# Performance work log

Hardware: AMD Instinct MI355X
Metric: run time of the kernel (lower is better)

The kernel has to match this reference:

```python
import jax, jax.numpy as jnp
import numpy as np

OSC_TIME = 10
UNITS = 256
D_IN = 256
BATCH = 32
SEQLEN = 2000


def setup_inputs() -> dict:
    key = jax.random.key(0)
    k1, k2, k3 = jax.random.split(key, 3)
    scale = 1.0 / np.sqrt(UNITS)
    x = jax.random.normal(k1, (BATCH, SEQLEN, D_IN), dtype=jnp.float32)
    W_x = jax.random.normal(k2, (4, 2, D_IN, UNITS), dtype=jnp.float32) * scale
    W_h = jax.random.normal(k3, (4, 2, UNITS, UNITS), dtype=jnp.float32) * scale
    b_x = jnp.zeros((4, 2, UNITS), dtype=jnp.float32)
    b_h = jnp.zeros((4, 2, UNITS), dtype=jnp.float32)
    return {"x": x, "W_x": W_x, "b_x": b_x, "W_h": W_h, "b_h": b_h}


def reference(x, W_x, b_x, W_h, b_h):
    # Subsample every OSC_TIME steps (tf.gather stride)
    xs = x[:, ::OSC_TIME]                       # [B, Ts, D]
    B, Ts, _ = xs.shape
    U = W_h.shape[-1]

    # Precompute input projections for all 4 cells x 2 gates: [4,2,B,Ts,U]
    xp = jnp.einsum('btd,cgdu->cgbtu', xs, W_x) + b_x[:, :, None, None, :]

    h0 = jnp.zeros((4, B, U), dtype=x.dtype)

    def ff_step(h, xp_t):                       # h [4,B,U], xp_t [4,2,B,U]
        hp = jnp.einsum('cbu,cguv->cgbv', h, W_h) + b_h[:, :, None, :]
        g = jax.nn.sigmoid(xp_t + hp)           # [4,2,B,U]
        j, k = g[:, 0], g[:, 1]
        h_new = j * (1.0 - h) + (1.0 - k) * h   # flip-flop update
        return h_new, h_new

    _, hs = jax.lax.scan(ff_step, h0, jnp.moveaxis(xp, 3, 0))  # hs [Ts,4,B,U]
    phi, omega, r, mu = hs[:, 0], hs[:, 1], hs[:, 2], hs[:, 3]  # each [Ts,B,U]

    # Oscillator: emit z = r*cos(phi) then update r, phi; OSC_TIME sub-steps
    def osc_step(carry, _):
        r_t, phi_t = carry
        z = r_t * jnp.cos(phi_t)
        r_n = r_t + (mu - jnp.square(r_t)) * r_t
        phi_n = phi_t + omega
        return (r_n, phi_n), z

    _, zs = jax.lax.scan(osc_step, (r, phi), None, length=OSC_TIME)  # [S,Ts,B,U]
    out = jnp.transpose(zs, (2, 1, 0, 3)).reshape(B, Ts * OSC_TIME, U)
    return out
```

## Files before the change

kernel.cpp:

```cpp
#include <hip/hip_runtime.h>
#include <hip/hip_fp16.h>
#include <stdint.h>

#define TS 200

typedef _Float16 h2_t  __attribute__((ext_vector_type(2)));
typedef _Float16 f16x8 __attribute__((ext_vector_type(8)));
typedef float    f32x4 __attribute__((ext_vector_type(4)));

static __device__ __forceinline__ float fdot2f(uint32_t w, uint32_t h, float acc) {
#if __has_builtin(__builtin_amdgcn_fdot2)
    return __builtin_amdgcn_fdot2(__builtin_bit_cast(h2_t, w),
                                  __builtin_bit_cast(h2_t, h), acc, false);
#else
    h2_t a = __builtin_bit_cast(h2_t, w), b = __builtin_bit_cast(h2_t, h);
    acc = fmaf((float)a.x, (float)b.x, acc);
    acc = fmaf((float)a.y, (float)b.y, acc);
    return acc;
#endif
}

template <int CTRL>
static __device__ __forceinline__ float dpp_add(float x) {
    int m = __builtin_amdgcn_update_dpp(0, __builtin_bit_cast(int, x), CTRL, 0xF, 0xF, true);
    return x + __builtin_bit_cast(float, m);
}
template <int CTRL>
static __device__ __forceinline__ float dpp_mov(float x) {
    int m = __builtin_amdgcn_update_dpp(0, __builtin_bit_cast(int, x), CTRL, 0xF, 0xF, true);
    return __builtin_bit_cast(float, m);
}

__global__ __launch_bounds__(256) void pack_all(const float* __restrict__ x,
                                                const float* __restrict__ Wx,
                                                const float* __restrict__ Wh,
                                                _Float16* __restrict__ xh,
                                                _Float16* __restrict__ wxt,
                                                uint32_t* __restrict__ wp) {
    int bid = blockIdx.x, tid = threadIdx.x;
    if (bid < 6400) {
        int row = bid, col = tid;
        int b = row / 200, t = row - b * 200;
        xh[(size_t)row * 256 + col] = (_Float16)x[((size_t)(b * 2000 + t * 10)) * 256 + col];
    } else if (bid < 8448) {
        int n = bid - 6400, k = tid;
        wxt[(size_t)n * 256 + k] = (_Float16)Wx[((size_t)((n >> 8) * 256 + k)) * 256 + (n & 255)];
    } else {
        int idx = (bid - 8448) * 256 + tid;
        int e   = idx & 3;
        int thr = (idx >> 2) & 1023;
        int j   = (idx >> 12) & 15;
        int c   = idx >> 16;
        int a = j >> 2, i = j & 3;
        int uu = a >> 1, g = a & 1;
        int vs = thr & 7, uq = (thr >> 3) & 7, wv = thr >> 6;
        int u = (wv * 8 + uq) * 2 + uu;
        int v = vs * 32 + i * 8 + e * 2;
        const float* base = Wh + ((size_t)((c * 2 + g) * 256 + v)) * 256 + u;
        h2_t p; p.x = (_Float16)base[0]; p.y = (_Float16)base[256];
        wp[idx] = __builtin_bit_cast(uint32_t, p);
    }
}

__global__ __launch_bounds__(256) void xp_gemm(const _Float16* __restrict__ xh,
                                               const _Float16* __restrict__ wxt,
                                               const float* __restrict__ bxf,
                                               _Float16* __restrict__ xp) {
    __shared__ _Float16 As[128 * 64];
    __shared__ _Float16 Bs[128 * 64];
    const int tid = threadIdx.x;
    const int lane = tid & 63, w = tid >> 6;
    const int m0 = (blockIdx.x >> 4) * 128;
    const int n0 = (blockIdx.x & 15) * 128;
    const int mw = (w & 1) * 64, nw = (w >> 1) * 64;

    f32x4 acc[4][4] = {};

    for (int kb = 0; kb < 4; kb++) {
        const int k0 = kb * 64;
#pragma unroll
        for (int q = 0; q < 4; q++) {
            int ii = w * 4 + q;
            int r = ii * 8 + (lane >> 3);
            int kcol = (lane & 7) * 8;
            const _Float16* ga = xh  + (size_t)(m0 + r) * 256 + k0 + kcol;
            const _Float16* gb = wxt + (size_t)(n0 + r) * 256 + k0 + kcol;
            __builtin_amdgcn_global_load_lds(
                (const __attribute__((address_space(1))) uint32_t*)ga,
                (__attribute__((address_space(3))) uint32_t*)(As + ii * 512), 16, 0, 0);
            __builtin_amdgcn_global_load_lds(
                (const __attribute__((address_space(1))) uint32_t*)gb,
                (__attribute__((address_space(3))) uint32_t*)(Bs + ii * 512), 16, 0, 0);
        }
        __syncthreads();
#pragma unroll
        for (int kc = 0; kc < 2; kc++) {
            f16x8 a[4], b[4];
#pragma unroll
            for (int mt = 0; mt < 4; mt++)
                a[mt] = *(const f16x8*)&As[(mw + mt * 16 + (lane & 15)) * 64 + kc * 32 + (lane >> 4) * 8];
#pragma unroll
            for (int nt = 0; nt < 4; nt++)
                b[nt] = *(const f16x8*)&Bs[(nw + nt * 16 + (lane & 15)) * 64 + kc * 32 + (lane >> 4) * 8];
#pragma unroll
            for (int mt = 0; mt < 4; mt++)
#pragma unroll
                for (int nt = 0; nt < 4; nt++)
                    acc[mt][nt] = __builtin_amdgcn_mfma_f32_16x16x32_f16(a[mt], b[nt], acc[mt][nt], 0, 0, 0);
        }
        __syncthreads();
    }

    const int nl = lane & 15, quad = lane >> 4;
#pragma unroll
    for (int nt = 0; nt < 4; nt++) {
        int n = n0 + nw + nt * 16 + nl;
        float bias = bxf[n];
        int c = n >> 9, gu = n & 511;
#pragma unroll
        for (int mt = 0; mt < 4; mt++)
#pragma unroll
            for (int r = 0; r < 4; r++) {
                int m = m0 + mw + mt * 16 + quad * 4 + r;
                int b = m / 200, t = m - b * 200;
                xp[((size_t)((c * 32 + b) * 200 + t)) * 512 + gu] =
                    (_Float16)(acc[mt][nt][r] + bias);
            }
    }
}

#define D4(ACC, W, H)                 \
    ACC = fdot2f(W.x, H.x, ACC);      \
    ACC = fdot2f(W.y, H.y, ACC);      \
    ACC = fdot2f(W.z, H.z, ACC);      \
    ACC = fdot2f(W.w, H.w, ACC);

#define PIN4(W) asm volatile("" : "+v"(W.x), "+v"(W.y), "+v"(W.z), "+v"(W.w))

__global__ __attribute__((amdgpu_flat_work_group_size(1024, 1024),
                          amdgpu_waves_per_eu(4, 4)))
void recurrence(const _Float16* __restrict__ xp,
                const float* __restrict__ bh,
                const uint32_t* __restrict__ Wp,
                float* __restrict__ hs) {
    const int cb  = blockIdx.x;
    const int c   = cb >> 5;
    const int tid = threadIdx.x;
    const int lane = tid & 63;
    const int vs = lane & 7;
    const int uq = lane >> 3;
    const int wv = tid >> 6;
    const int upair = wv * 8 + uq;
    const int u0 = upair * 2;

    __shared__ __align__(16) uint32_t h2s[2][160];

    const uint4* wb = (const uint4*)Wp + (size_t)c * 16 * 1024 + tid;
    uint4 w00 = wb[0 * 1024],  w01 = wb[1 * 1024],  w02 = wb[2 * 1024],  w03 = wb[3 * 1024];
    uint4 w10 = wb[4 * 1024],  w11 = wb[5 * 1024],  w12 = wb[6 * 1024],  w13 = wb[7 * 1024];
    uint4 w20 = wb[8 * 1024],  w21 = wb[9 * 1024],  w22 = wb[10 * 1024], w23 = wb[11 * 1024];
    uint4 w30 = wb[12 * 1024], w31 = wb[13 * 1024], w32 = wb[14 * 1024], w33 = wb[15 * 1024];
    PIN4(w00); PIN4(w01); PIN4(w02); PIN4(w03);
    PIN4(w10); PIN4(w11); PIN4(w12); PIN4(w13);
    PIN4(w20); PIN4(w21); PIN4(w22); PIN4(w23);
    PIN4(w30); PIN4(w31); PIN4(w32); PIN4(w33);

    float bias = 0.f;
    const _Float16* xpb = nullptr;
    if (vs < 4) {
        int g_sel = vs & 1, u_sel = u0 + (vs >> 1);
        bias = bh[(c * 2 + g_sel) * 256 + u_sel];
        xpb  = xp + (size_t)cb * 200 * 512 + g_sel * 256 + u_sel;
    }

    float hreg = 0.f;
    if (tid < 160) { h2s[0][tid] = 0u; }
    __syncthreads();

    float* hsb = hs + (size_t)cb * 200 * 256 + u0;

    for (int t = 0; t < TS; t++) {
        const uint32_t* hbuf = h2s[t & 1];
        uint32_t* hnext = h2s[(t + 1) & 1];

        float xpv = 0.f;
        if (vs < 4) xpv = (float)xpb[(size_t)t * 512];

        uint4 h0 = *(const uint4*)(hbuf + vs * 20 + 0);
        uint4 h1 = *(const uint4*)(hbuf + vs * 20 + 4);
        uint4 h2 = *(const uint4*)(hbuf + vs * 20 + 8);
        uint4 h3 = *(const uint4*)(hbuf + vs * 20 + 12);

        float acc0 = 0.f, acc1 = 0.f, acc2 = 0.f, acc3 = 0.f;
        D4(acc0, w00, h0) D4(acc1, w10, h0) D4(acc2, w20, h0) D4(acc3, w30, h0)
        D4(acc0, w01, h1) D4(acc1, w11, h1) D4(acc2, w21, h1) D4(acc3, w31, h1)
        D4(acc0, w02, h2) D4(acc1, w12, h2) D4(acc2, w22, h2) D4(acc3, w32, h2)
        D4(acc0, w03, h3) D4(acc1, w13, h3) D4(acc2, w23, h3) D4(acc3, w33, h3)

        acc0 = dpp_add<0x141>(dpp_add<0x4E>(dpp_add<0xB1>(acc0)));
        acc1 = dpp_add<0x141>(dpp_add<0x4E>(dpp_add<0xB1>(acc1)));
        acc2 = dpp_add<0x141>(dpp_add<0x4E>(dpp_add<0xB1>(acc2)));
        acc3 = dpp_add<0x141>(dpp_add<0x4E>(dpp_add<0xB1>(acc3)));

        float s = (vs == 0) ? acc0 : (vs == 1) ? acc1 : (vs == 2) ? acc2 : acc3;
        s += xpv + bias;
        float sig = 1.f / (1.f + __expf(-s));
        float kg = dpp_mov<0xB1>(sig);
        float hn = sig + hreg * (1.f - sig - kg);
        hreg = hn;
        float hn1 = dpp_mov<0x4E>(hn);
        if (vs == 0) {
            h2_t p; p.x = (_Float16)hn; p.y = (_Float16)hn1;
            hnext[(upair >> 4) * 20 + (upair & 15)] = __builtin_bit_cast(uint32_t, p);
            *(float2*)(hsb + (size_t)t * 256) = make_float2(hn, hn1);
        }
        __syncthreads();
    }
}

__global__ __launch_bounds__(256) void osc(const float* __restrict__ hs,
                                           float* __restrict__ out) {
    int tid = blockIdx.x * 256 + threadIdx.x;
    const int cstride = 32 * 200 * 256;
    int u = tid & 255;
    int bt = tid >> 8;
    int t = bt % 200, b = bt / 200;
    float phi   = hs[0 * cstride + tid];
    float omega = hs[1 * cstride + tid];
    float r     = hs[2 * cstride + tid];
    float mu    = hs[3 * cstride + tid];
    float* o = out + ((size_t)(b * 2000 + t * 10)) * 256 + u;
#pragma unroll
    for (int s = 0; s < 10; s++) {
        o[(size_t)s * 256] = r * __cosf(phi);
        r = r + (mu - r * r) * r;
        phi = phi + omega;
    }
}

extern "C" void kernel_launch(void* const* d_in, const int* in_sizes, int n_in,
                              void* d_out, int out_size, void* d_ws, size_t ws_size,
                              hipStream_t stream) {
    const float* x  = (const float*)d_in[0];
    const float* Wx = (const float*)d_in[1];
    const float* bx = (const float*)d_in[2];
    const float* Wh = (const float*)d_in[3];
    const float* bh = (const float*)d_in[4];
    float* out = (float*)d_out;

    char* ws = (char*)d_ws;
    const size_t XP = (size_t)4 * 32 * 200 * 512 * 2;
    const size_t HS = (size_t)4 * 32 * 200 * 256 * 4;
    const size_t XH = (size_t)6400 * 256 * 2;

    _Float16* xp  = (_Float16*)ws;
    float*    hs  = (float*)(ws + XP);
    _Float16* xh  = (_Float16*)(ws + XP);
    _Float16* wxt = (_Float16*)(ws + XP + XH);
    uint32_t* wp  = (uint32_t*)(ws + XP + HS);

    pack_all<<<9472, 256, 0, stream>>>(x, Wx, Wh, xh, wxt, wp);
    xp_gemm<<<800, 256, 0, stream>>>(xh, wxt, bx, xp);
    recurrence<<<128, 1024, 0, stream>>>(xp, bh, wp, hs);
    osc<<<6400, 256, 0, stream>>>(hs, out);
}
```

Measured before the change: 374.0 us.

## Halve recurrence block size, each thread computes two unit-pairs

The recurrence kernel now launches 512 threads per block instead of 1024, and each thread holds two sets of weight registers (A and B halves, 128 units apart). Each thread does twice the dot-product work per timestep. The aim is to reduce per-step barrier cost and wave count across the serial loop, and to add ILP by interleaving independent accumulations. In exchange, register pressure doubles, with 128 pinned weight VGPRs plus accumulators, which could cause spills or lower occupancy limits.

```diff
diff --git a/kernel.cpp b/kernel.cpp
--- a/kernel.cpp
+++ b/kernel.cpp
@@ -137,8 +137,8 @@
 
 #define PIN4(W) asm volatile("" : "+v"(W.x), "+v"(W.y), "+v"(W.z), "+v"(W.w))
 
-__global__ __attribute__((amdgpu_flat_work_group_size(1024, 1024),
-                          amdgpu_waves_per_eu(4, 4)))
+__global__ __attribute__((amdgpu_flat_work_group_size(512, 512),
+                          amdgpu_waves_per_eu(2, 2)))
 void recurrence(const _Float16* __restrict__ xp,
                 const float* __restrict__ bh,
                 const uint32_t* __restrict__ Wp,
@@ -150,30 +150,39 @@
     const int vs = lane & 7;
     const int uq = lane >> 3;
     const int wv = tid >> 6;
-    const int upair = wv * 8 + uq;
-    const int u0 = upair * 2;
+    const int up0 = wv * 8 + uq;
+    const int u0 = up0 * 2;
 
     __shared__ __align__(16) uint32_t h2s[2][160];
 
     const uint4* wb = (const uint4*)Wp + (size_t)c * 16 * 1024 + tid;
-    uint4 w00 = wb[0 * 1024],  w01 = wb[1 * 1024],  w02 = wb[2 * 1024],  w03 = wb[3 * 1024];
-    uint4 w10 = wb[4 * 1024],  w11 = wb[5 * 1024],  w12 = wb[6 * 1024],  w13 = wb[7 * 1024];
-    uint4 w20 = wb[8 * 1024],  w21 = wb[9 * 1024],  w22 = wb[10 * 1024], w23 = wb[11 * 1024];
-    uint4 w30 = wb[12 * 1024], w31 = wb[13 * 1024], w32 = wb[14 * 1024], w33 = wb[15 * 1024];
-    PIN4(w00); PIN4(w01); PIN4(w02); PIN4(w03);
-    PIN4(w10); PIN4(w11); PIN4(w12); PIN4(w13);
-    PIN4(w20); PIN4(w21); PIN4(w22); PIN4(w23);
-    PIN4(w30); PIN4(w31); PIN4(w32); PIN4(w33);
-
-    float bias = 0.f;
+    uint4 wA00 = wb[0 * 1024],        wA01 = wb[1 * 1024],        wA02 = wb[2 * 1024],        wA03 = wb[3 * 1024];
+    uint4 wA10 = wb[4 * 1024],        wA11 = wb[5 * 1024],        wA12 = wb[6 * 1024],        wA13 = wb[7 * 1024];
+    uint4 wA20 = wb[8 * 1024],        wA21 = wb[9 * 1024],        wA22 = wb[10 * 1024],       wA23 = wb[11 * 1024];
+    uint4 wA30 = wb[12 * 1024],       wA31 = wb[13 * 1024],       wA32 = wb[14 * 1024],       wA33 = wb[15 * 1024];
+    uint4 wB00 = wb[0 * 1024 + 512],  wB01 = wb[1 * 1024 + 512],  wB02 = wb[2 * 1024 + 512],  wB03 = wb[3 * 1024 + 512];
+    uint4 wB10 = wb[4 * 1024 + 512],  wB11 = wb[5 * 1024 + 512],  wB12 = wb[6 * 1024 + 512],  wB13 = wb[7 * 1024 + 512];
+    uint4 wB20 = wb[8 * 1024 + 512],  wB21 = wb[9 * 1024 + 512],  wB22 = wb[10 * 1024 + 512], wB23 = wb[11 * 1024 + 512];
+    uint4 wB30 = wb[12 * 1024 + 512], wB31 = wb[13 * 1024 + 512], wB32 = wb[14 * 1024 + 512], wB33 = wb[15 * 1024 + 512];
+    PIN4(wA00); PIN4(wA01); PIN4(wA02); PIN4(wA03);
+    PIN4(wA10); PIN4(wA11); PIN4(wA12); PIN4(wA13);
+    PIN4(wA20); PIN4(wA21); PIN4(wA22); PIN4(wA23);
+    PIN4(wA30); PIN4(wA31); PIN4(wA32); PIN4(wA33);
+    PIN4(wB00); PIN4(wB01); PIN4(wB02); PIN4(wB03);
+    PIN4(wB10); PIN4(wB11); PIN4(wB12); PIN4(wB13);
+    PIN4(wB20); PIN4(wB21); PIN4(wB22); PIN4(wB23);
+    PIN4(wB30); PIN4(wB31); PIN4(wB32); PIN4(wB33);
+
+    float biasA = 0.f, biasB = 0.f;
     const _Float16* xpb = nullptr;
     if (vs < 4) {
         int g_sel = vs & 1, u_sel = u0 + (vs >> 1);
-        bias = bh[(c * 2 + g_sel) * 256 + u_sel];
+        biasA = bh[(c * 2 + g_sel) * 256 + u_sel];
+        biasB = bh[(c * 2 + g_sel) * 256 + u_sel + 128];
         xpb  = xp + (size_t)cb * 200 * 512 + g_sel * 256 + u_sel;
     }
 
-    float hreg = 0.f;
+    float hregA = 0.f, hregB = 0.f;
     if (tid < 160) { h2s[0][tid] = 0u; }
     __syncthreads();
 
@@ -183,36 +192,59 @@
         const uint32_t* hbuf = h2s[t & 1];
         uint32_t* hnext = h2s[(t + 1) & 1];
 
-        float xpv = 0.f;
-        if (vs < 4) xpv = (float)xpb[(size_t)t * 512];
+        float xpA = 0.f, xpB = 0.f;
+        if (vs < 4) {
+            xpA = (float)xpb[(size_t)t * 512];
+            xpB = (float)xpb[(size_t)t * 512 + 128];
+        }
 
         uint4 h0 = *(const uint4*)(hbuf + vs * 20 + 0);
         uint4 h1 = *(const uint4*)(hbuf + vs * 20 + 4);
         uint4 h2 = *(const uint4*)(hbuf + vs * 20 + 8);
         uint4 h3 = *(const uint4*)(hbuf + vs * 20 + 12);
 
-        float acc0 = 0.f, acc1 = 0.f, acc2 = 0.f, acc3 = 0.f;
-        D4(acc0, w00, h0) D4(acc1, w10, h0) D4(acc2, w20, h0) D4(acc3, w30, h0)
-        D4(acc0, w01, h1) D4(acc1, w11, h1) D4(acc2, w21, h1) D4(acc3, w31, h1)
-        D4(acc0, w02, h2) D4(acc1, w12, h2) D4(acc2, w22, h2) D4(acc3, w32, h2)
-        D4(acc0, w03, h3) D4(acc1, w13, h3) D4(acc2, w23, h3) D4(acc3, w33, h3)
-
-        acc0 = dpp_add<0x141>(dpp_add<0x4E>(dpp_add<0xB1>(acc0)));
-        acc1 = dpp_add<0x141>(dpp_add<0x4E>(dpp_add<0xB1>(acc1)));
-        acc2 = dpp_add<0x141>(dpp_add<0x4E>(dpp_add<0xB1>(acc2)));
-        acc3 = dpp_add<0x141>(dpp_add<0x4E>(dpp_add<0xB1>(acc3)));
-
-        float s = (vs == 0) ? acc0 : (vs == 1) ? acc1 : (vs == 2) ? acc2 : acc3;
-        s += xpv + bias;
-        float sig = 1.f / (1.f + __expf(-s));
-        float kg = dpp_mov<0xB1>(sig);
-        float hn = sig + hreg * (1.f - sig - kg);
-        hreg = hn;
-        float hn1 = dpp_mov<0x4E>(hn);
+        float aA0 = 0.f, aA1 = 0.f, aA2 = 0.f, aA3 = 0.f;
+        float aB0 = 0.f, aB1 = 0.f, aB2 = 0.f, aB3 = 0.f;
+        D4(aA0, wA00, h0) D4(aB0, wB00, h0) D4(aA1, wA10, h0) D4(aB1, wB10, h0)
+        D4(aA2, wA20, h0) D4(aB2, wB20, h0) D4(aA3, wA30, h0) D4(aB3, wB30, h0)
+        D4(aA0, wA01, h1) D4(aB0, wB01, h1) D4(aA1, wA11, h1) D4(aB1, wB11, h1)
+        D4(aA2, wA21, h1) D4(aB2, wB21, h1) D4(aA3, wA31, h1) D4(aB3, wB31, h1)
+        D4(aA0, wA02, h2) D4(aB0, wB02, h2) D4(aA1, wA12, h2) D4(aB1, wB12, h2)
+        D4(aA2, wA22, h2) D4(aB2, wB22, h2) D4(aA3, wA32, h2) D4(aB3, wB32, h2)
+        D4(aA0, wA03, h3) D4(aB0, wB03, h3) D4(aA1, wA13, h3) D4(aB1, wB13, h3)
+        D4(aA2, wA23, h3) D4(aB2, wB23, h3) D4(aA3, wA33, h3) D4(aB3, wB33, h3)
+
+        aA0 = dpp_add<0x141>(dpp_add<0x4E>(dpp_add<0xB1>(aA0)));
+        aA1 = dpp_add<0x141>(dpp_add<0x4E>(dpp_add<0xB1>(aA1)));
+        aA2 = dpp_add<0x141>(dpp_add<0x4E>(dpp_add<0xB1>(aA2)));
+        aA3 = dpp_add<0x141>(dpp_add<0x4E>(dpp_add<0xB1>(aA3)));
+        aB0 = dpp_add<0x141>(dpp_add<0x4E>(dpp_add<0xB1>(aB0)));
+        aB1 = dpp_add<0x141>(dpp_add<0x4E>(dpp_add<0xB1>(aB1)));
+        aB2 = dpp_add<0x141>(dpp_add<0x4E>(dpp_add<0xB1>(aB2)));
+        aB3 = dpp_add<0x141>(dpp_add<0x4E>(dpp_add<0xB1>(aB3)));
+
+        float sA = (vs == 0) ? aA0 : (vs == 1) ? aA1 : (vs == 2) ? aA2 : aA3;
+        float sB = (vs == 0) ? aB0 : (vs == 1) ? aB1 : (vs == 2) ? aB2 : aB3;
+        sA += xpA + biasA;
+        sB += xpB + biasB;
+        float sigA = 1.f / (1.f + __expf(-sA));
+        float sigB = 1.f / (1.f + __expf(-sB));
+        float kgA = dpp_mov<0xB1>(sigA);
+        float kgB = dpp_mov<0xB1>(sigB);
+        float hnA = sigA + hregA * (1.f - sigA - kgA);
+        float hnB = sigB + hregB * (1.f - sigB - kgB);
+        hregA = hnA;
+        hregB = hnB;
+        float hn1A = dpp_mov<0x4E>(hnA);
+        float hn1B = dpp_mov<0x4E>(hnB);
         if (vs == 0) {
-            h2_t p; p.x = (_Float16)hn; p.y = (_Float16)hn1;
-            hnext[(upair >> 4) * 20 + (upair & 15)] = __builtin_bit_cast(uint32_t, p);
-            *(float2*)(hsb + (size_t)t * 256) = make_float2(hn, hn1);
+            h2_t pA; pA.x = (_Float16)hnA; pA.y = (_Float16)hn1A;
+            h2_t pB; pB.x = (_Float16)hnB; pB.y = (_Float16)hn1B;
+            int idx0 = (up0 >> 4) * 20 + (up0 & 15);
+            hnext[idx0]      = __builtin_bit_cast(uint32_t, pA);
+            hnext[idx0 + 80] = __builtin_bit_cast(uint32_t, pB);
+            *(float2*)(hsb + (size_t)t * 256)       = make_float2(hnA, hn1A);
+            *(float2*)(hsb + (size_t)t * 256 + 128) = make_float2(hnB, hn1B);
         }
         __syncthreads();
     }
@@ -261,6 +293,6 @@
 
     pack_all<<<9472, 256, 0, stream>>>(x, Wx, Wh, xh, wxt, wp);
     xp_gemm<<<800, 256, 0, stream>>>(xh, wxt, bx, xp);
-    recurrence<<<128, 1024, 0, stream>>>(xp, bh, wp, hs);
+    recurrence<<<128, 512, 0, stream>>>(xp, bh, wp, hs);
     osc<<<6400, 256, 0, stream>>>(hs, out);
 }
```

Measured after the change: 381.2 us. About the same (+1.9%).

## Batch recurrence across 16 sequences per workgroup using MFMA with register-resident weights

Applied to the files above, without the earlier changes.

The recurrence kernel now processes 16 batch rows per workgroup. Each step's h·W_h product runs as 16x16x32 f16 MFMA tiles against weights pinned in registers, replacing per-sequence fdot2 dot products with DPP reductions. The h state is exchanged through XOR-swizzled LDS, the next step's xp values are prefetched, and the barrier becomes a lighter LDS-only one. Weight packing is rewritten to the MFMA operand layout. The grid shrinks from 128 to 8 workgroups, trading parallelism across CUs for far fewer weight loads and matrix-core throughput, so per-step latency on only 8 CUs may dominate.

```diff
diff --git a/kernel.cpp b/kernel.cpp
--- a/kernel.cpp
+++ b/kernel.cpp
@@ -7,28 +7,11 @@
 typedef _Float16 h2_t  __attribute__((ext_vector_type(2)));
 typedef _Float16 f16x8 __attribute__((ext_vector_type(8)));
 typedef float    f32x4 __attribute__((ext_vector_type(4)));
-
-static __device__ __forceinline__ float fdot2f(uint32_t w, uint32_t h, float acc) {
-#if __has_builtin(__builtin_amdgcn_fdot2)
-    return __builtin_amdgcn_fdot2(__builtin_bit_cast(h2_t, w),
-                                  __builtin_bit_cast(h2_t, h), acc, false);
-#else
-    h2_t a = __builtin_bit_cast(h2_t, w), b = __builtin_bit_cast(h2_t, h);
-    acc = fmaf((float)a.x, (float)b.x, acc);
-    acc = fmaf((float)a.y, (float)b.y, acc);
-    return acc;
-#endif
-}
 
 template <int CTRL>
 static __device__ __forceinline__ float dpp_add(float x) {
     int m = __builtin_amdgcn_update_dpp(0, __builtin_bit_cast(int, x), CTRL, 0xF, 0xF, true);
     return x + __builtin_bit_cast(float, m);
-}
-template <int CTRL>
-static __device__ __forceinline__ float dpp_mov(float x) {
-    int m = __builtin_amdgcn_update_dpp(0, __builtin_bit_cast(int, x), CTRL, 0xF, 0xF, true);
-    return __builtin_bit_cast(float, m);
 }
 
 __global__ __launch_bounds__(256) void pack_all(const float* __restrict__ x,
@@ -36,7 +19,7 @@
                                                 const float* __restrict__ Wh,
                                                 _Float16* __restrict__ xh,
                                                 _Float16* __restrict__ wxt,
-                                                uint32_t* __restrict__ wp) {
+                                                _Float16* __restrict__ wp) {
     int bid = blockIdx.x, tid = threadIdx.x;
     if (bid < 6400) {
         int row = bid, col = tid;
@@ -46,19 +29,17 @@
         int n = bid - 6400, k = tid;
         wxt[(size_t)n * 256 + k] = (_Float16)Wx[((size_t)((n >> 8) * 256 + k)) * 256 + (n & 255)];
     } else {
-        int idx = (bid - 8448) * 256 + tid;
-        int e   = idx & 3;
-        int thr = (idx >> 2) & 1023;
-        int j   = (idx >> 12) & 15;
-        int c   = idx >> 16;
-        int a = j >> 2, i = j & 3;
-        int uu = a >> 1, g = a & 1;
-        int vs = thr & 7, uq = (thr >> 3) & 7, wv = thr >> 6;
-        int u = (wv * 8 + uq) * 2 + uu;
-        int v = vs * 32 + i * 8 + e * 2;
-        const float* base = Wh + ((size_t)((c * 2 + g) * 256 + v)) * 256 + u;
-        h2_t p; p.x = (_Float16)base[0]; p.y = (_Float16)base[256];
-        wp[idx] = __builtin_bit_cast(uint32_t, p);
+        int i = (bid - 8448) * 256 + tid;
+        int e  = i & 7;
+        int ln = (i >> 3) & 63;
+        int kt = (i >> 9) & 7;
+        int nt = (i >> 12) & 3;
+        int w  = (i >> 14) & 7;
+        int c  = i >> 17;
+        int g = nt >> 1, par = nt & 1;
+        int u = w * 32 + 2 * (ln & 15) + par;
+        int k = kt * 32 + (ln >> 4) * 8 + e;
+        wp[i] = (_Float16)Wh[((size_t)((c * 2 + g) * 256 + k)) * 256 + u];
     }
 }
 
@@ -129,92 +110,130 @@
     }
 }
 
-#define D4(ACC, W, H)                 \
-    ACC = fdot2f(W.x, H.x, ACC);      \
-    ACC = fdot2f(W.y, H.y, ACC);      \
-    ACC = fdot2f(W.z, H.z, ACC);      \
-    ACC = fdot2f(W.w, H.w, ACC);
-
 #define PIN4(W) asm volatile("" : "+v"(W.x), "+v"(W.y), "+v"(W.z), "+v"(W.w))
 
-__global__ __attribute__((amdgpu_flat_work_group_size(1024, 1024),
-                          amdgpu_waves_per_eu(4, 4)))
+#define LDS_BARRIER()                                        \
+    do {                                                     \
+        __builtin_amdgcn_sched_barrier(0);                   \
+        asm volatile("s_waitcnt lgkmcnt(0)" ::: "memory");   \
+        __builtin_amdgcn_s_barrier();                        \
+        __builtin_amdgcn_sched_barrier(0);                   \
+    } while (0)
+
+__global__ __attribute__((amdgpu_flat_work_group_size(512, 512),
+                          amdgpu_waves_per_eu(2, 2)))
 void recurrence(const _Float16* __restrict__ xp,
                 const float* __restrict__ bh,
-                const uint32_t* __restrict__ Wp,
+                const _Float16* __restrict__ Wp,
                 float* __restrict__ hs) {
-    const int cb  = blockIdx.x;
-    const int c   = cb >> 5;
+    const int wg  = blockIdx.x;
+    const int c   = wg >> 1;
+    const int bb  = wg & 1;
     const int tid = threadIdx.x;
     const int lane = tid & 63;
-    const int vs = lane & 7;
-    const int uq = lane >> 3;
-    const int wv = tid >> 6;
-    const int upair = wv * 8 + uq;
-    const int u0 = upair * 2;
-
-    __shared__ __align__(16) uint32_t h2s[2][160];
-
-    const uint4* wb = (const uint4*)Wp + (size_t)c * 16 * 1024 + tid;
-    uint4 w00 = wb[0 * 1024],  w01 = wb[1 * 1024],  w02 = wb[2 * 1024],  w03 = wb[3 * 1024];
-    uint4 w10 = wb[4 * 1024],  w11 = wb[5 * 1024],  w12 = wb[6 * 1024],  w13 = wb[7 * 1024];
-    uint4 w20 = wb[8 * 1024],  w21 = wb[9 * 1024],  w22 = wb[10 * 1024], w23 = wb[11 * 1024];
-    uint4 w30 = wb[12 * 1024], w31 = wb[13 * 1024], w32 = wb[14 * 1024], w33 = wb[15 * 1024];
-    PIN4(w00); PIN4(w01); PIN4(w02); PIN4(w03);
-    PIN4(w10); PIN4(w11); PIN4(w12); PIN4(w13);
-    PIN4(w20); PIN4(w21); PIN4(w22); PIN4(w23);
-    PIN4(w30); PIN4(w31); PIN4(w32); PIN4(w33);
-
-    float bias = 0.f;
-    const _Float16* xpb = nullptr;
-    if (vs < 4) {
-        int g_sel = vs & 1, u_sel = u0 + (vs >> 1);
-        bias = bh[(c * 2 + g_sel) * 256 + u_sel];
-        xpb  = xp + (size_t)cb * 200 * 512 + g_sel * 256 + u_sel;
-    }
-
-    float hreg = 0.f;
-    if (tid < 160) { h2s[0][tid] = 0u; }
+    const int w    = tid >> 6;
+    const int c16  = lane & 15;
+    const int quad = lane >> 4;
+    const int ub   = w * 32;
+
+    __shared__ __align__(16) char hb[2][16 * 512];
+
+    uint4 W[4][8];
+    {
+        const uint4* wq = (const uint4*)Wp;
+        const int base = ((c * 8 + w) * 4) * 8 * 64;
+#pragma unroll
+        for (int nt = 0; nt < 4; nt++)
+#pragma unroll
+            for (int kt = 0; kt < 8; kt++)
+                W[nt][kt] = wq[base + (nt * 8 + kt) * 64 + lane];
+    }
+#pragma unroll
+    for (int nt = 0; nt < 4; nt++)
+#pragma unroll
+        for (int kt = 0; kt < 8; kt++) { PIN4(W[nt][kt]); }
+
+    float bias[4];
+    int   guo[4];
+#pragma unroll
+    for (int nt = 0; nt < 4; nt++) {
+        int g = nt >> 1, par = nt & 1;
+        int u = ub + 2 * c16 + par;
+        bias[nt] = bh[(c * 2 + g) * 256 + u];
+        guo[nt]  = g * 256 + u;
+    }
+    const size_t cb0 = (size_t)(c * 32 + bb * 16 + quad * 4);
+
+    ((float4*)hb[0])[tid] = make_float4(0.f, 0.f, 0.f, 0.f);
+    float hE[4] = {0.f, 0.f, 0.f, 0.f};
+    float hO[4] = {0.f, 0.f, 0.f, 0.f};
+
+    float cur[4][4];
+#pragma unroll
+    for (int nt = 0; nt < 4; nt++)
+#pragma unroll
+        for (int r = 0; r < 4; r++)
+            cur[nt][r] = (float)xp[(cb0 + r) * 102400 + guo[nt]];
+
     __syncthreads();
 
-    float* hsb = hs + (size_t)cb * 200 * 256 + u0;
-
     for (int t = 0; t < TS; t++) {
-        const uint32_t* hbuf = h2s[t & 1];
-        uint32_t* hnext = h2s[(t + 1) & 1];
-
-        float xpv = 0.f;
-        if (vs < 4) xpv = (float)xpb[(size_t)t * 512];
-
-        uint4 h0 = *(const uint4*)(hbuf + vs * 20 + 0);
-        uint4 h1 = *(const uint4*)(hbuf + vs * 20 + 4);
-        uint4 h2 = *(const uint4*)(hbuf + vs * 20 + 8);
-        uint4 h3 = *(const uint4*)(hbuf + vs * 20 + 12);
-
-        float acc0 = 0.f, acc1 = 0.f, acc2 = 0.f, acc3 = 0.f;
-        D4(acc0, w00, h0) D4(acc1, w10, h0) D4(acc2, w20, h0) D4(acc3, w30, h0)
-        D4(acc0, w01, h1) D4(acc1, w11, h1) D4(acc2, w21, h1) D4(acc3, w31, h1)
-        D4(acc0, w02, h2) D4(acc1, w12, h2) D4(acc2, w22, h2) D4(acc3, w32, h2)
-        D4(acc0, w03, h3) D4(acc1, w13, h3) D4(acc2, w23, h3) D4(acc3, w33, h3)
-
-        acc0 = dpp_add<0x141>(dpp_add<0x4E>(dpp_add<0xB1>(acc0)));
-        acc1 = dpp_add<0x141>(dpp_add<0x4E>(dpp_add<0xB1>(acc1)));
-        acc2 = dpp_add<0x141>(dpp_add<0x4E>(dpp_add<0xB1>(acc2)));
-        acc3 = dpp_add<0x141>(dpp_add<0x4E>(dpp_add<0xB1>(acc3)));
-
-        float s = (vs == 0) ? acc0 : (vs == 1) ? acc1 : (vs == 2) ? acc2 : acc3;
-        s += xpv + bias;
-        float sig = 1.f / (1.f + __expf(-s));
-        float kg = dpp_mov<0xB1>(sig);
-        float hn = sig + hreg * (1.f - sig - kg);
-        hreg = hn;
-        float hn1 = dpp_mov<0x4E>(hn);
-        if (vs == 0) {
-            h2_t p; p.x = (_Float16)hn; p.y = (_Float16)hn1;
-            hnext[(upair >> 4) * 20 + (upair & 15)] = __builtin_bit_cast(uint32_t, p);
-            *(float2*)(hsb + (size_t)t * 256) = make_float2(hn, hn1);
-        }
-        __syncthreads();
+        const char* rbuf = hb[t & 1];
+        char* wbuf = hb[(t + 1) & 1];
+
+        _Float16 nxt[4][4];
+        if (t + 1 < TS) {
+#pragma unroll
+            for (int nt = 0; nt < 4; nt++)
+#pragma unroll
+                for (int r = 0; r < 4; r++)
+                    nxt[nt][r] = xp[(cb0 + r) * 102400 + (size_t)(t + 1) * 512 + guo[nt]];
+        }
+
+        f32x4 acc[4] = {};
+        const int bA = c16;
+#pragma unroll
+        for (int kt = 0; kt < 8; kt++) {
+            int off = bA * 512 + ((kt * 64 + quad * 16) ^ ((bA & 7) << 4));
+            f16x8 a = *(const f16x8*)(rbuf + off);
+#pragma unroll
+            for (int nt = 0; nt < 4; nt++)
+                acc[nt] = __builtin_amdgcn_mfma_f32_16x16x32_f16(
+                    a, __builtin_bit_cast(f16x8, W[nt][kt]), acc[nt], 0, 0, 0);
+        }
+
+#pragma unroll
+        for (int r = 0; r < 4; r++) {
+            float sJE = acc[0][r] + cur[0][r] + bias[0];
+            float sJO = acc[1][r] + cur[1][r] + bias[1];
+            float sKE = acc[2][r] + cur[2][r] + bias[2];
+            float sKO = acc[3][r] + cur[3][r] + bias[3];
+            float jE = 1.f / (1.f + __expf(-sJE));
+            float jO = 1.f / (1.f + __expf(-sJO));
+            float kE = 1.f / (1.f + __expf(-sKE));
+            float kO = 1.f / (1.f + __expf(-sKO));
+            float hEn = jE + hE[r] * (1.f - jE - kE);
+            float hOn = jO + hO[r] * (1.f - jO - kO);
+            hE[r] = hEn; hO[r] = hOn;
+
+            int b = quad * 4 + r;
+            int woff = b * 512 + ((w * 64 + c16 * 4) ^ ((b & 7) << 4));
+            h2_t p; p.x = (_Float16)hEn; p.y = (_Float16)hOn;
+            *(uint32_t*)(wbuf + woff) = __builtin_bit_cast(uint32_t, p);
+
+            *(float2*)(hs + (cb0 + r) * 51200 + (size_t)t * 256 + ub + 2 * c16) =
+                make_float2(hEn, hOn);
+        }
+
+        if (t + 1 < TS) {
+#pragma unroll
+            for (int nt = 0; nt < 4; nt++)
+#pragma unroll
+                for (int r = 0; r < 4; r++)
+                    cur[nt][r] = (float)nxt[nt][r];
+        }
+
+        LDS_BARRIER();
     }
 }
 
@@ -257,10 +276,10 @@
     float*    hs  = (float*)(ws + XP);
     _Float16* xh  = (_Float16*)(ws + XP);
     _Float16* wxt = (_Float16*)(ws + XP + XH);
-    uint32_t* wp  = (uint32_t*)(ws + XP + HS);
-
-    pack_all<<<9472, 256, 0, stream>>>(x, Wx, Wh, xh, wxt, wp);
+    _Float16* wp  = (_Float16*)(ws + XP + HS);
+
+    pack_all<<<10496, 256, 0, stream>>>(x, Wx, Wh, xh, wxt, wp);
     xp_gemm<<<800, 256, 0, stream>>>(xh, wxt, bx, xp);
-    recurrence<<<128, 1024, 0, stream>>>(xp, bh, wp, hs);
+    recurrence<<<8, 512, 0, stream>>>(xp, bh, wp, hs);
     osc<<<6400, 256, 0, stream>>>(hs, out);
 }
```

After: 473.9 us. +26.7%, slower.
